# Performance work log

Hardware: AMD Instinct MI355X
Metric: run time of the kernel (lower is better)

Reference implementation:

```python
import jax, jax.numpy as jnp
import numpy as np

N_A, N_G, D, H = 100000, 25000, 128, 4
E_B, E_O, E_R, E_P = 400000, 100000, 200000, 200000
BN_INV = float(1.0 / np.sqrt(1.0 + 1e-5))  # eval-mode BatchNorm1d, running mean 0 / var 1


def setup_inputs():
    key = jax.random.key(0)
    ks = iter(jax.random.split(key, 64))
    nrm = lambda shape, s=0.05: jax.random.normal(next(ks), shape, jnp.float32) * s
    ri = lambda n, hi: jax.random.randint(next(ks), (n,), 0, hi, jnp.int32)
    inp = dict(
        x_atom=nrm((N_A, D), 1.0), x_group=nrm((N_G, D), 1.0),
        ef_bond=nrm((E_B, D), 1.0), ef_overlap=nrm((E_O, D), 1.0),
        bond_src=ri(E_B, N_A), bond_dst=ri(E_B, N_A),
        ov_src=ri(E_O, N_G), ov_dst=ri(E_O, N_G),
        ref_src=ri(E_R, N_G), ref_dst=ri(E_R, N_A),
        pool_src=ri(E_P, N_A), pool_dst=ri(E_P, N_G),
    )
    # two GINE convs (bond 'b', overlap 'o'): eps + MLP Linear(D,2D)->BN->ReLU->Linear(2D,D)
    for pre in ('b', 'o'):
        inp[pre + '_eps'] = jnp.zeros((1,), jnp.float32)
        inp[pre + '_W1'] = nrm((D, 2 * D)); inp[pre + '_b1'] = jnp.zeros((2 * D,), jnp.float32)
        inp[pre + '_g1'] = jnp.ones((2 * D,), jnp.float32); inp[pre + '_be1'] = jnp.zeros((2 * D,), jnp.float32)
        inp[pre + '_W2'] = nrm((2 * D, D)); inp[pre + '_b2'] = jnp.zeros((D,), jnp.float32)
    # two ModifiedGATConvs (refine 'r', pool 'p'): GATConv + Flatten->BN->ReLU->Linear
    for pre in ('r', 'p'):
        inp[pre + '_Wfc'] = nrm((D, H * D)); inp[pre + '_al'] = nrm((H, D)); inp[pre + '_ar'] = nrm((H, D))
        inp[pre + '_Wres'] = nrm((D, H * D)); inp[pre + '_bias'] = jnp.zeros((H * D,), jnp.float32)
        inp[pre + '_g'] = jnp.ones((H * D,), jnp.float32); inp[pre + '_b'] = jnp.zeros((H * D,), jnp.float32)
        inp[pre + '_Wout'] = nrm((H * D, D)); inp[pre + '_bout'] = jnp.zeros((D,), jnp.float32)
    return inp


def _gine(x_src, x_dst, efeat, src, dst, n_dst, eps, W1, b1, g1, be1, W2, b2):
    m = jax.nn.relu(x_src[src] + efeat)                       # [E, D] message: relu(h_src + e)
    neigh = jax.ops.segment_sum(m, dst, num_segments=n_dst)   # [Nd, D] sum-reduce
    h = (1.0 + eps) * x_dst + neigh
    h = h @ W1 + b1
    h = jax.nn.relu(g1 * (h * BN_INV) + be1)                  # eval BN
    return h @ W2 + b2


def _gat(x_src, x_dst, src, dst, n_dst, Wfc, al, ar, Wres, bias, g, b, Wout, bout):
    hs = (x_src @ Wfc).reshape(-1, H, D)                      # [Ns, H, D]
    hd = (x_dst @ Wfc).reshape(-1, H, D)
    el = jnp.sum(hs * al, axis=-1)                            # [Ns, H]
    er = jnp.sum(hd * ar, axis=-1)                            # [Nd, H]
    e = jax.nn.leaky_relu(el[src] + er[dst], 0.2)             # [E, H]
    emax = jax.ops.segment_max(e, dst, num_segments=n_dst)    # per-dst softmax (stable)
    ex = jnp.exp(e - emax[dst])
    den = jax.ops.segment_sum(ex, dst, num_segments=n_dst)
    a = ex / jnp.maximum(den[dst], 1e-9)                      # [E, H]
    rst = jax.ops.segment_sum(a[:, :, None] * hs[src], dst, num_segments=n_dst)  # [Nd, H, D]
    rst = rst + (x_dst @ Wres).reshape(-1, H, D) + bias.reshape(H, D)            # residual + bias
    flat = rst.reshape(-1, H * D)                             # Flatten
    h = jax.nn.relu(g * (flat * BN_INV) + b)                  # eval BN -> ReLU
    return h @ Wout + bout


def reference(x_atom, x_group, ef_bond, ef_overlap, bond_src, bond_dst, ov_src, ov_dst, ref_src, ref_dst, pool_src, pool_dst, b_eps, b_W1, b_b1, b_g1, b_be1, b_W2, b_b2, o_eps, o_W1, o_b1, o_g1, o_be1, o_W2, o_b2, r_Wfc, r_al, r_ar, r_Wres, r_bias, r_g, r_b, r_Wout, r_bout, p_Wfc, p_al, p_ar, p_Wres, p_bias, p_g, p_b, p_Wout, p_bout):
    # HeteroGraphConv with default 'sum' cross-relation aggregation per dst node type
    out_atom = _gine(x_atom, x_atom, ef_bond, bond_src, bond_dst, N_A, b_eps, b_W1, b_b1, b_g1, b_be1, b_W2, b_b2)
    out_atom = out_atom + _gat(x_group, x_atom, ref_src, ref_dst, N_A, r_Wfc, r_al, r_ar, r_Wres, r_bias, r_g, r_b, r_Wout, r_bout)
    out_group = _gine(x_group, x_group, ef_overlap, ov_src, ov_dst, N_G, o_eps, o_W1, o_b1, o_g1, o_be1, o_W2, o_b2)
    out_group = out_group + _gat(x_atom, x_group, pool_src, pool_dst, N_G, p_Wfc, p_al, p_ar, p_Wres, p_bias, p_g, p_b, p_Wout, p_bout)
    return jnp.concatenate([out_atom, out_group], axis=0)     # [N_A + N_G, D]
```

## Files before the change

### kernel.cpp

```cpp
#include <hip/hip_runtime.h>
#include <hip/hip_bf16.h>

#define N_A 100000
#define N_G 25000
#define DD 128
#define E_B 400000
#define E_O 100000
#define E_R 200000
#define E_P 200000
#define EALL 900000
#define NSLOT 250000
#define STRIDE 64
#define NALL 125000
#define GBN 7813

static constexpr float BN_INV_C = 0.99999500003749969f;

typedef __attribute__((ext_vector_type(8))) short bf16x8;
typedef __attribute__((ext_vector_type(4))) float f32x4;

__device__ __forceinline__ unsigned short f2bf(float f) {
    unsigned u = __float_as_uint(f);
    unsigned r = (u + 0x7FFFu + ((u >> 16) & 1u)) >> 16;
    return (unsigned short)r;
}
__device__ __forceinline__ float bf2f(unsigned short s) {
    return __uint_as_float(((unsigned)s) << 16);
}
__device__ __forceinline__ float lrelu(float v) { return v > 0.f ? v : 0.2f * v; }

__device__ __forceinline__ void gload16(const unsigned short* g, unsigned short* l) {
    __builtin_amdgcn_global_load_lds(
        (const __attribute__((address_space(1))) void*)g,
        (__attribute__((address_space(3))) void*)l, 16, 0, 0);
}

struct WcSeg { const float* src; unsigned short* dst; int K; int N; int ldk; int off; };
struct PrepArgs {
    const float* xa; const float* xg;
    unsigned short* xab; unsigned short* xgb;
    WcSeg wc[10];
    const float* rWfc; const float* ral; const float* rar;
    const float* pWfc; const float* pal; const float* par;
    float* wv;
    const int* bs; const int* bd; const int* os; const int* od;
    const int* rs; const int* rd; const int* ps; const int* pd;
    int* deg; uint2* adj; int* heads; int* nxt;
};

#define PB_XC 15625
#define PB_WC 2560
#define PB_WAR 8

__global__ __launch_bounds__(256) void k_prep(PrepArgs p) {
    int bx = blockIdx.x, tid = threadIdx.x;
    if (bx < PB_XC) {
        int t = bx * 256 + tid;
        if (t < N_A * 32) {
            float4 v = *(const float4*)(p.xa + (size_t)t * 4);
            ushort4 o; o.x = f2bf(v.x); o.y = f2bf(v.y); o.z = f2bf(v.z); o.w = f2bf(v.w);
            *(ushort4*)(p.xab + (size_t)t * 4) = o;
        } else {
            int t2 = t - N_A * 32;
            if (t2 < N_G * 32) {
                float4 v = *(const float4*)(p.xg + (size_t)t2 * 4);
                ushort4 o; o.x = f2bf(v.x); o.y = f2bf(v.y); o.z = f2bf(v.z); o.w = f2bf(v.w);
                *(ushort4*)(p.xgb + (size_t)t2 * 4) = o;
            }
        }
    } else if (bx < PB_XC + PB_WC) {
        int b2 = bx - PB_XC;
        WcSeg sg = p.wc[b2 >> 8];
        int t = ((b2 & 255) << 8) + tid;
        if (t < sg.K * sg.N) {
            int n = t % sg.N, k = t / sg.N;
            sg.dst[(size_t)n * sg.ldk + sg.off + k] = f2bf(sg.src[t]);
        }
    } else if (bx < PB_XC + PB_WC + PB_WAR) {
        int b3 = bx - (PB_XC + PB_WC);
        int bsel = b3 >> 1;
        int t = ((b3 & 1) << 8) + tid;
        const float* W = bsel < 2 ? p.rWfc : p.pWfc;
        const float* vec = bsel == 0 ? p.ral : bsel == 1 ? p.rar : bsel == 2 ? p.pal : p.par;
        int k = t >> 2, h = t & 3;
        const float* wr = W + (size_t)k * 512 + h * 128;
        const float* av = vec + h * 128;
        float s = 0.f;
        for (int d = 0; d < 128; ++d) s += wr[d] * av[d];
        p.wv[bsel * 512 + t] = s;
    } else {
        int t = (bx - (PB_XC + PB_WC + PB_WAR)) * 256 + tid;
        int e, base, go; const int* S; const int* D;
        if (t < E_B) { e = t; S = p.bs; D = p.bd; base = 0; go = 0; }
        else if (t < E_B + E_O) { e = t - E_B; S = p.os; D = p.od; base = 100000; go = E_B; }
        else if (t < E_B + E_O + E_R) { e = t - (E_B + E_O); S = p.rs; D = p.rd; base = 125000; go = E_B + E_O; }
        else if (t < EALL) { e = t - (E_B + E_O + E_R); S = p.ps; D = p.pd; base = 225000; go = E_B + E_O + E_R; }
        else return;
        int d = D[e], s = S[e];
        int ns = base + d;
        int pos = atomicAdd(&p.deg[ns], 1);
        if (pos < STRIDE) p.adj[(size_t)ns * STRIDE + pos] = make_uint2((unsigned)e, (unsigned)s);
        else p.nxt[go + e] = atomicExch(&p.heads[ns], e);
    }
}

__device__ __forceinline__ void gine16_body(
    int bx, int tid,
    const unsigned short* __restrict__ xAb, const unsigned short* __restrict__ xGb,
    const float* __restrict__ efB, const float* __restrict__ efO,
    const int* __restrict__ bsrc, const int* __restrict__ osrc,
    const int* __restrict__ deg, const uint2* __restrict__ adj,
    const int* __restrict__ heads, const int* __restrict__ nxt,
    const float* __restrict__ beps, const float* __restrict__ oeps,
    unsigned short* __restrict__ h0A, unsigned short* __restrict__ h0G,
    uint2* glbuf, int* degb) {
    int wid = tid >> 6, lane = tid & 63;
    int half = lane >> 5, l32 = lane & 31;
    int nbase = bx * 16 + wid * 4;
    bool atomside = nbase < N_A;
    const unsigned short* xs = atomside ? xAb : xGb;
    const float* ef = atomside ? efB : efO;
    const int* esrc = atomside ? bsrc : osrc;
    const int* nx = atomside ? nxt : nxt + E_B;
    float ep = 1.0f + (atomside ? beps[0] : oeps[0]);
    unsigned short* h0 = atomside ? h0A : h0G;
    uint2* glw = glbuf + wid * 4 * STRIDE;
#pragma unroll
    for (int j = 0; j < 4; ++j) {
        int nj = nbase + j;
        if (nj < NALL) glw[j * STRIDE + lane] = adj[(size_t)nj * STRIDE + lane];
    }
    if (lane < 4) {
        int nj = nbase + lane;
        degb[wid * 4 + lane] = (nj < NALL) ? deg[nj] : 0;
    }
    __syncthreads();
    for (int j = 0; j < 4; ++j) {
        int nj = nbase + j;
        if (nj >= NALL) break;
        int dd = degb[wid * 4 + j];
        int cb = min(dd, STRIDE);
        int nn = atomside ? nj : nj - N_A;
        const uint2* gl = glw + j * STRIDE;
        float4 acc = make_float4(0.f, 0.f, 0.f, 0.f);
        int i = 0;
        for (; i + 4 <= cb; i += 4) {
            uint2 eA = gl[i + half];
            uint2 eB = gl[i + 2 + half];
            uint2 xwA = *(const uint2*)(xs + (size_t)eA.y * DD + l32 * 4);
            float4 evA = *(const float4*)(ef + (size_t)eA.x * DD + l32 * 4);
            uint2 xwB = *(const uint2*)(xs + (size_t)eB.y * DD + l32 * 4);
            float4 evB = *(const float4*)(ef + (size_t)eB.x * DD + l32 * 4);
            acc.x += fmaxf(bf2f((unsigned short)(xwA.x & 0xffff)) + evA.x, 0.f);
            acc.y += fmaxf(bf2f((unsigned short)(xwA.x >> 16)) + evA.y, 0.f);
            acc.z += fmaxf(bf2f((unsigned short)(xwA.y & 0xffff)) + evA.z, 0.f);
            acc.w += fmaxf(bf2f((unsigned short)(xwA.y >> 16)) + evA.w, 0.f);
            acc.x += fmaxf(bf2f((unsigned short)(xwB.x & 0xffff)) + evB.x, 0.f);
            acc.y += fmaxf(bf2f((unsigned short)(xwB.x >> 16)) + evB.y, 0.f);
            acc.z += fmaxf(bf2f((unsigned short)(xwB.y & 0xffff)) + evB.z, 0.f);
            acc.w += fmaxf(bf2f((unsigned short)(xwB.y >> 16)) + evB.w, 0.f);
        }
        for (; i + 2 <= cb; i += 2) {
            uint2 eA = gl[i + half];
            uint2 xwA = *(const uint2*)(xs + (size_t)eA.y * DD + l32 * 4);
            float4 evA = *(const float4*)(ef + (size_t)eA.x * DD + l32 * 4);
            acc.x += fmaxf(bf2f((unsigned short)(xwA.x & 0xffff)) + evA.x, 0.f);
            acc.y += fmaxf(bf2f((unsigned short)(xwA.x >> 16)) + evA.y, 0.f);
            acc.z += fmaxf(bf2f((unsigned short)(xwA.y & 0xffff)) + evA.z, 0.f);
            acc.w += fmaxf(bf2f((unsigned short)(xwA.y >> 16)) + evA.w, 0.f);
        }
        if (i < cb && half == 0) {
            uint2 eA = gl[i];
            uint2 xwA = *(const uint2*)(xs + (size_t)eA.y * DD + l32 * 4);
            float4 evA = *(const float4*)(ef + (size_t)eA.x * DD + l32 * 4);
            acc.x += fmaxf(bf2f((unsigned short)(xwA.x & 0xffff)) + evA.x, 0.f);
            acc.y += fmaxf(bf2f((unsigned short)(xwA.x >> 16)) + evA.y, 0.f);
            acc.z += fmaxf(bf2f((unsigned short)(xwA.y & 0xffff)) + evA.z, 0.f);
            acc.w += fmaxf(bf2f((unsigned short)(xwA.y >> 16)) + evA.w, 0.f);
        }
        if (dd > STRIDE && half == 0) {
            for (int e = heads[nj]; e >= 0; e = nx[e]) {
                int s = esrc[e];
                uint2 xwA = *(const uint2*)(xs + (size_t)s * DD + l32 * 4);
                float4 evA = *(const float4*)(ef + (size_t)e * DD + l32 * 4);
                acc.x += fmaxf(bf2f((unsigned short)(xwA.x & 0xffff)) + evA.x, 0.f);
                acc.y += fmaxf(bf2f((unsigned short)(xwA.x >> 16)) + evA.y, 0.f);
                acc.z += fmaxf(bf2f((unsigned short)(xwA.y & 0xffff)) + evA.z, 0.f);
                acc.w += fmaxf(bf2f((unsigned short)(xwA.y >> 16)) + evA.w, 0.f);
            }
        }
        acc.x += __shfl_xor(acc.x, 32, 64);
        acc.y += __shfl_xor(acc.y, 32, 64);
        acc.z += __shfl_xor(acc.z, 32, 64);
        acc.w += __shfl_xor(acc.w, 32, 64);
        uint2 xd = *(const uint2*)(xs + (size_t)nn * DD + l32 * 4);
        float r0 = ep * bf2f((unsigned short)(xd.x & 0xffff)) + acc.x;
        float r1 = ep * bf2f((unsigned short)(xd.x >> 16)) + acc.y;
        float r2 = ep * bf2f((unsigned short)(xd.y & 0xffff)) + acc.z;
        float r3 = ep * bf2f((unsigned short)(xd.y >> 16)) + acc.w;
        if (half == 0) {
            uint2 o;
            o.x = (unsigned)f2bf(r0) | ((unsigned)f2bf(r1) << 16);
            o.y = (unsigned)f2bf(r2) | ((unsigned)f2bf(r3) << 16);
            *(uint2*)(h0 + (size_t)nn * DD + l32 * 4) = o;
        }
    }
}

__device__ __forceinline__ void logit_body(
    int t,
    const unsigned short* __restrict__ xAb, const unsigned short* __restrict__ xGb,
    const float* __restrict__ wv,
    float* __restrict__ elR, float* __restrict__ elP,
    float* __restrict__ erR, float* __restrict__ erP) {
    const unsigned short* xr; const float* wl; const float* wr_; float* ol; float* orr; int idx;
    if (t < N_A * 4) {
        idx = t; xr = xAb + (size_t)(t >> 2) * DD; wl = wv + 1024; wr_ = wv + 512;
        ol = elP; orr = erR;
    } else {
        int t2 = t - N_A * 4;
        if (t2 >= N_G * 4) return;
        idx = t2; xr = xGb + (size_t)(t2 >> 2) * DD; wl = wv; wr_ = wv + 1536;
        ol = elR; orr = erP;
    }
    int h = idx & 3;
    float sl = 0.f, sr = 0.f;
#pragma unroll
    for (int k = 0; k < DD; k += 8) {
        uint4 w = *(const uint4*)(xr + k);
        unsigned wa[4] = {w.x, w.y, w.z, w.w};
#pragma unroll
        for (int q = 0; q < 4; ++q) {
            float x0 = bf2f((unsigned short)(wa[q] & 0xffff));
            float x1 = bf2f((unsigned short)(wa[q] >> 16));
            int k0 = (k + q * 2) * 4 + h, k1 = (k + q * 2 + 1) * 4 + h;
            sl += x0 * wl[k0] + x1 * wl[k1];
            sr += x0 * wr_[k0] + x1 * wr_[k1];
        }
    }
    ol[idx] = sl;
    orr[idx] = sr;
}

__global__ __launch_bounds__(256) void k_gather_logit(
    const unsigned short* __restrict__ xAb, const unsigned short* __restrict__ xGb,
    const float* __restrict__ efB, const float* __restrict__ efO,
    const int* __restrict__ bsrc, const int* __restrict__ osrc,
    const int* __restrict__ deg, const uint2* __restrict__ adj,
    const int* __restrict__ heads, const int* __restrict__ nxt,
    const float* __restrict__ beps, const float* __restrict__ oeps,
    unsigned short* __restrict__ h0A, unsigned short* __restrict__ h0G,
    const float* __restrict__ wv,
    float* __restrict__ elR, float* __restrict__ elP,
    float* __restrict__ erR, float* __restrict__ erP) {
    __shared__ uint2 gl[16 * STRIDE];
    __shared__ int degb[16];
    int bx = blockIdx.x;
    if (bx < GBN)
        gine16_body(bx, threadIdx.x, xAb, xGb, efB, efO, bsrc, osrc, deg, adj, heads, nxt,
                    beps, oeps, h0A, h0G, gl, degb);
    else
        logit_body((bx - GBN) * 256 + threadIdx.x, xAb, xGb, wv, elR, elP, erR, erP);
}

__device__ __forceinline__ void exp_body(
    int t,
    const float* __restrict__ elR, const float* __restrict__ erR,
    const float* __restrict__ elP, const float* __restrict__ erP,
    const int* __restrict__ rs, const int* __restrict__ rd,
    const int* __restrict__ ps, const int* __restrict__ pd,
    float* __restrict__ exR, float* __restrict__ exP,
    float* __restrict__ denR, float* __restrict__ denP) {
    if (t < E_R * 4) {
        int e = t >> 2, h = t & 3;
        float v = lrelu(elR[rs[e] * 4 + h] + erR[rd[e] * 4 + h]);
        float x = __expf(v);
        exR[t] = x;
        atomicAdd(&denR[rd[e] * 4 + h], x);
    } else {
        int t2 = t - E_R * 4;
        if (t2 >= E_P * 4) return;
        int e = t2 >> 2, h = t2 & 3;
        float v = lrelu(elP[ps[e] * 4 + h] + erP[pd[e] * 4 + h]);
        float x = __expf(v);
        exP[t2] = x;
        atomicAdd(&denP[pd[e] * 4 + h], x);
    }
}

__global__ __launch_bounds__(256) void k_att_gather_all(
    const unsigned short* __restrict__ xAb, const unsigned short* __restrict__ xGb,
    const float* __restrict__ exR, const float* __restrict__ exP,
    const float* __restrict__ denR, const float* __restrict__ denP,
    const int* __restrict__ rsrc, const int* __restrict__ psrc,
    const int* __restrict__ deg, const uint2* __restrict__ adj,
    const int* __restrict__ heads, const int* __restrict__ nxt,
    unsigned short* __restrict__ A2r, unsigned short* __restrict__ A2p) {
    __shared__ uint2 glbuf[16 * STRIDE];
    __shared__ int degb[16];
    int tid = threadIdx.x;
    int wid = tid >> 6, lane = tid & 63;
    int half = lane >> 5, l32 = lane & 31;
    int nbase = blockIdx.x * 16 + wid * 4;
    bool atomside = nbase < N_A;
    const unsigned short* xs = atomside ? xGb : xAb;
    const float* ex = atomside ? exR : exP;
    const float* den = atomside ? denR : denP;
    const int* esrc = atomside ? rsrc : psrc;
    const int* nx = atomside ? nxt + (E_B + E_O) : nxt + (E_B + E_O + E_R);
    unsigned short* A2b = atomside ? A2r : A2p;
    uint2* glw = glbuf + wid * 4 * STRIDE;
#pragma unroll
    for (int j = 0; j < 4; ++j) {
        int nj = nbase + j;
        if (nj < NALL) glw[j * STRIDE + lane] = adj[(size_t)(125000 + nj) * STRIDE + lane];
    }
    if (lane < 4) {
        int nj = nbase + lane;
        degb[wid * 4 + lane] = (nj < NALL) ? deg[125000 + nj] : 0;
    }
    __syncthreads();
    for (int j = 0; j < 4; ++j) {
        int nj = nbase + j;
        if (nj >= NALL) break;
        int dd = degb[wid * 4 + j];
        int cb = min(dd, STRIDE);
        int nn = atomside ? nj : nj - N_A;
        const uint2* gl = glw + j * STRIDE;
        unsigned short* A2 = A2b + (size_t)nn * 512;
        float4 dv = *(const float4*)(den + (size_t)nn * 4);
        float inv0 = 1.f / fmaxf(dv.x, 1e-9f);
        float inv1 = 1.f / fmaxf(dv.y, 1e-9f);
        float inv2 = 1.f / fmaxf(dv.z, 1e-9f);
        float inv3 = 1.f / fmaxf(dv.w, 1e-9f);
        float acc[4][4] = {};
        int i = 0;
#define ATT_EDGE(e4_, xw_) { \
        float x0 = bf2f((unsigned short)(xw_.x & 0xffff)); \
        float x1 = bf2f((unsigned short)(xw_.x >> 16)); \
        float x2 = bf2f((unsigned short)(xw_.y & 0xffff)); \
        float x3 = bf2f((unsigned short)(xw_.y >> 16)); \
        float a0 = e4_.x * inv0, a1 = e4_.y * inv1, a2 = e4_.z * inv2, a3 = e4_.w * inv3; \
        acc[0][0] += a0 * x0; acc[0][1] += a0 * x1; acc[0][2] += a0 * x2; acc[0][3] += a0 * x3; \
        acc[1][0] += a1 * x0; acc[1][1] += a1 * x1; acc[1][2] += a1 * x2; acc[1][3] += a1 * x3; \
        acc[2][0] += a2 * x0; acc[2][1] += a2 * x1; acc[2][2] += a2 * x2; acc[2][3] += a2 * x3; \
        acc[3][0] += a3 * x0; acc[3][1] += a3 * x1; acc[3][2] += a3 * x2; acc[3][3] += a3 * x3; }
        for (; i + 4 <= cb; i += 4) {
            uint2 eA = gl[i + half], eB = gl[i + 2 + half];
            float4 e4A = *(const float4*)(ex + (size_t)eA.x * 4);
            uint2 xwA = *(const uint2*)(xs + (size_t)eA.y * DD + l32 * 4);
            float4 e4B = *(const float4*)(ex + (size_t)eB.x * 4);
            uint2 xwB = *(const uint2*)(xs + (size_t)eB.y * DD + l32 * 4);
            ATT_EDGE(e4A, xwA);
            ATT_EDGE(e4B, xwB);
        }
        for (; i + 2 <= cb; i += 2) {
            uint2 eA = gl[i + half];
            float4 e4A = *(const float4*)(ex + (size_t)eA.x * 4);
            uint2 xwA = *(const uint2*)(xs + (size_t)eA.y * DD + l32 * 4);
            ATT_EDGE(e4A, xwA);
        }
        if (i < cb && half == 0) {
            uint2 eA = gl[i];
            float4 e4A = *(const float4*)(ex + (size_t)eA.x * 4);
            uint2 xwA = *(const uint2*)(xs + (size_t)eA.y * DD + l32 * 4);
            ATT_EDGE(e4A, xwA);
        }
        if (dd > STRIDE && half == 0) {
            for (int e = heads[125000 + nj]; e >= 0; e = nx[e]) {
                int s = esrc[e];
                float4 e4A = *(const float4*)(ex + (size_t)e * 4);
                uint2 xwA = *(const uint2*)(xs + (size_t)s * DD + l32 * 4);
                ATT_EDGE(e4A, xwA);
            }
        }
#undef ATT_EDGE
#pragma unroll
        for (int h = 0; h < 4; ++h)
#pragma unroll
            for (int q = 0; q < 4; ++q)
                acc[h][q] += __shfl_xor(acc[h][q], 32, 64);
        if (half == 0) {
#pragma unroll
            for (int h = 0; h < 4; ++h) {
                uint2 o;
                o.x = (unsigned)f2bf(acc[h][0]) | ((unsigned)f2bf(acc[h][1]) << 16);
                o.y = (unsigned)f2bf(acc[h][2]) | ((unsigned)f2bf(acc[h][3]) << 16);
                *(uint2*)(A2 + h * 128 + l32 * 4) = o;
            }
        }
    }
}

template <int EPI, int OUTBF, int GATK>
__device__ __forceinline__ void gemm_body(
    const unsigned short* __restrict__ A, const unsigned short* __restrict__ Bt,
    void* __restrict__ C, int M, int N, int K,
    const float* __restrict__ bias, const float* __restrict__ g,
    const float* __restrict__ be, const unsigned short* __restrict__ addbf,
    const unsigned short* __restrict__ Axd, int bxx, int byy,
    unsigned short* As, unsigned short* Bs) {
    int tid = threadIdx.x;
    int wave = tid >> 6, lane = tid & 63;
    int wr = wave >> 1, wc = wave & 1;
    int row0 = byy * 128, col0 = bxx * 128;
    int l16 = lane & 15, q = lane >> 4;
    int r0s = wave * 16 + (lane >> 2);
    int r1s = r0s + 64;
    int swl = (lane ^ (lane >> 2) ^ (lane >> 4)) & 3;
    int swr = (l16 ^ (l16 >> 2)) & 3;
    unsigned short* ldsA0 = As + wave * 512;
    unsigned short* ldsA1 = As + 2048 + wave * 512;
    unsigned short* ldsB0 = Bs + wave * 512;
    unsigned short* ldsB1 = Bs + 2048 + wave * 512;
    f32x4 acc[4][4] = {};
    for (int k0 = 0; k0 < K; k0 += 32) {
        __syncthreads();
        {
            int kk = k0 + swl * 8;
            int ra0 = min(row0 + r0s, M - 1);
            int ra1 = min(row0 + r1s, M - 1);
            const unsigned short *pa0, *pa1;
            if (GATK) {
                if (k0 < 128) {
                    pa0 = A + (size_t)ra0 * 512 + col0 + kk;
                    pa1 = A + (size_t)ra1 * 512 + col0 + kk;
                } else {
                    pa0 = Axd + (size_t)ra0 * 128 + (kk - 128);
                    pa1 = Axd + (size_t)ra1 * 128 + (kk - 128);
                }
            } else {
                pa0 = A + (size_t)ra0 * K + kk;
                pa1 = A + (size_t)ra1 * K + kk;
            }
            gload16(pa0, ldsA0);
            gload16(pa1, ldsA1);
            gload16(Bt + (size_t)(col0 + r0s) * K + kk, ldsB0);
            gload16(Bt + (size_t)(col0 + r1s) * K + kk, ldsB1);
        }
        __syncthreads();
        bf16x8 af[4], bfr[4];
#pragma unroll
        for (int i = 0; i < 4; ++i) {
            int row = wr * 64 + i * 16 + l16;
            af[i] = *(const bf16x8*)(&As[row * 32 + ((q ^ swr) * 8)]);
        }
#pragma unroll
        for (int j = 0; j < 4; ++j) {
            int row = wc * 64 + j * 16 + l16;
            bfr[j] = *(const bf16x8*)(&Bs[row * 32 + ((q ^ swr) * 8)]);
        }
#pragma unroll
        for (int i = 0; i < 4; ++i)
#pragma unroll
            for (int j = 0; j < 4; ++j)
                acc[i][j] = __builtin_amdgcn_mfma_f32_16x16x32_bf16(af[i], bfr[j], acc[i][j], 0, 0, 0);
    }
    int rq = (lane >> 4) * 4;
#pragma unroll
    for (int i = 0; i < 4; ++i) {
#pragma unroll
        for (int reg = 0; reg < 4; ++reg) {
            int r = row0 + wr * 64 + i * 16 + rq + reg;
            if (r >= M) continue;
#pragma unroll
            for (int j = 0; j < 4; ++j) {
                int c = col0 + wc * 64 + j * 16 + l16;
                float v = acc[i][j][reg];
                size_t idx = (size_t)r * N + c;
                v += bias[c];
                if (EPI == 2) {
                    v = g[c] * (v * BN_INV_C) + be[c];
                    v = fmaxf(v, 0.f);
                }
                if (EPI == 3) {
                    ((float*)C)[idx] = v + bf2f(addbf[idx]);
                } else if (OUTBF) {
                    ((unsigned short*)C)[idx] = f2bf(v);
                } else {
                    ((float*)C)[idx] = v;
                }
            }
        }
    }
}

#define NBA 782
#define NBG 196

__global__ __launch_bounds__(256) void k_gemm1_exp(
    const unsigned short* h0A, const unsigned short* h0G,
    const unsigned short* WtB1, const unsigned short* WtO1,
    const float* bb1, const float* bg1, const float* bbe1,
    const float* ob1, const float* og1, const float* obe1,
    unsigned short* R4a, unsigned short* R4g,
    const float* elR, const float* erR, const float* elP, const float* erP,
    const int* rs, const int* rd, const int* ps, const int* pd,
    float* exR, float* exP, float* denR, float* denP) {
    __shared__ unsigned short As[4096];
    __shared__ unsigned short Bs[4096];
    int b = blockIdx.x;
    if (b < 2 * NBA)
        gemm_body<2, 1, 0>(h0A, WtB1, R4a, N_A, 256, 128, bb1, bg1, bbe1, nullptr, nullptr,
                           b & 1, b >> 1, As, Bs);
    else if (b < 2 * NBA + 2 * NBG) {
        int b2 = b - 2 * NBA;
        gemm_body<2, 1, 0>(h0G, WtO1, R4g, N_G, 256, 128, ob1, og1, obe1, nullptr, nullptr,
                           b2 & 1, b2 >> 1, As, Bs);
    } else {
        int t = (b - (2 * NBA + 2 * NBG)) * 256 + threadIdx.x;
        exp_body(t, elR, erR, elP, erP, rs, rd, ps, pd, exR, exP, denR, denP);
    }
}

__global__ __launch_bounds__(256) void k_gatk_mid(
    const unsigned short* R4a, const unsigned short* R4g,
    const unsigned short* WtB2, const unsigned short* WtO2,
    const float* bb2, const float* ob2,
    unsigned short* G1a, unsigned short* G1g,
    const unsigned short* A2r, const unsigned short* A2p,
    const unsigned short* xAb, const unsigned short* xGb,
    const unsigned short* WtR, const unsigned short* WtP,
    const float* rbias, const float* rg, const float* rb,
    const float* pbias, const float* pg, const float* pb,
    unsigned short* R3r, unsigned short* R3p) {
    __shared__ unsigned short As[4096];
    __shared__ unsigned short Bs[4096];
    int b = blockIdx.x;
    if (b < NBA)
        gemm_body<1, 1, 0>(R4a, WtB2, G1a, N_A, 128, 256, bb2, nullptr, nullptr, nullptr, nullptr,
                           0, b, As, Bs);
    else if (b < NBA + NBG)
        gemm_body<1, 1, 0>(R4g, WtO2, G1g, N_G, 128, 256, ob2, nullptr, nullptr, nullptr, nullptr,
                           0, b - NBA, As, Bs);
    else if (b < NBA + NBG + 4 * NBA) {
        int b3 = b - (NBA + NBG);
        gemm_body<2, 1, 1>(A2r, WtR, R3r, N_A, 512, 256, rbias, rg, rb, nullptr, xAb,
                           b3 & 3, b3 >> 2, As, Bs);
    } else {
        int b4 = b - (NBA + NBG + 4 * NBA);
        gemm_body<2, 1, 1>(A2p, WtP, R3p, N_G, 512, 256, pbias, pg, pb, nullptr, xGb,
                           b4 & 3, b4 >> 2, As, Bs);
    }
}

__global__ __launch_bounds__(256) void k_gemm_out(
    const unsigned short* R3r, const unsigned short* R3p,
    const unsigned short* WtRo, const unsigned short* WtPo,
    const float* rbout, const float* pbout,
    const unsigned short* G1a, const unsigned short* G1g,
    float* out) {
    __shared__ unsigned short As[4096];
    __shared__ unsigned short Bs[4096];
    int b = blockIdx.x;
    if (b < NBA)
        gemm_body<3, 0, 0>(R3r, WtRo, out, N_A, 128, 512, rbout, nullptr, nullptr, G1a, nullptr,
                           0, b, As, Bs);
    else
        gemm_body<3, 0, 0>(R3p, WtPo, out + (size_t)N_A * DD, N_G, 128, 512, pbout, nullptr, nullptr,
                           G1g, nullptr, 0, b - NBA, As, Bs);
}

extern "C" void kernel_launch(void* const* d_in, const int* in_sizes, int n_in,
                              void* d_out, int out_size, void* d_ws, size_t ws_size,
                              hipStream_t stream) {
    const float* x_atom = (const float*)d_in[0];
    const float* x_group = (const float*)d_in[1];
    const float* ef_bond = (const float*)d_in[2];
    const float* ef_ov = (const float*)d_in[3];
    const int* bond_src = (const int*)d_in[4];
    const int* bond_dst = (const int*)d_in[5];
    const int* ov_src = (const int*)d_in[6];
    const int* ov_dst = (const int*)d_in[7];
    const int* ref_src = (const int*)d_in[8];
    const int* ref_dst = (const int*)d_in[9];
    const int* pool_src = (const int*)d_in[10];
    const int* pool_dst = (const int*)d_in[11];
    const float* b_eps = (const float*)d_in[12];
    const float* b_W1 = (const float*)d_in[13];
    const float* b_b1 = (const float*)d_in[14];
    const float* b_g1 = (const float*)d_in[15];
    const float* b_be1 = (const float*)d_in[16];
    const float* b_W2 = (const float*)d_in[17];
    const float* b_b2 = (const float*)d_in[18];
    const float* o_eps = (const float*)d_in[19];
    const float* o_W1 = (const float*)d_in[20];
    const float* o_b1 = (const float*)d_in[21];
    const float* o_g1 = (const float*)d_in[22];
    const float* o_be1 = (const float*)d_in[23];
    const float* o_W2 = (const float*)d_in[24];
    const float* o_b2 = (const float*)d_in[25];
    const float* r_Wfc = (const float*)d_in[26];
    const float* r_al = (const float*)d_in[27];
    const float* r_ar = (const float*)d_in[28];
    const float* r_Wres = (const float*)d_in[29];
    const float* r_bias = (const float*)d_in[30];
    const float* r_g = (const float*)d_in[31];
    const float* r_b = (const float*)d_in[32];
    const float* r_Wout = (const float*)d_in[33];
    const float* r_bout = (const float*)d_in[34];
    const float* p_Wfc = (const float*)d_in[35];
    const float* p_al = (const float*)d_in[36];
    const float* p_ar = (const float*)d_in[37];
    const float* p_Wres = (const float*)d_in[38];
    const float* p_bias = (const float*)d_in[39];
    const float* p_g = (const float*)d_in[40];
    const float* p_b = (const float*)d_in[41];
    const float* p_Wout = (const float*)d_in[42];
    const float* p_bout = (const float*)d_in[43];

    float* out = (float*)d_out;
    char* wsb = (char*)d_ws;
    unsigned short* xAb = (unsigned short*)(wsb + 0);
    unsigned short* xGb = (unsigned short*)(wsb + 26000000);
    unsigned short* WtB1 = (unsigned short*)(wsb + 33000000);
    unsigned short* WtB2 = WtB1 + 32768;
    unsigned short* WtO1 = WtB2 + 32768;
    unsigned short* WtO2 = WtO1 + 32768;
    unsigned short* WtR  = WtO2 + 32768;
    unsigned short* WtRo = WtR + 131072;
    unsigned short* WtP  = WtRo + 65536;
    unsigned short* WtPo = WtP + 131072;
    float* wv   = (float*)(wsb + 34100000);
    int* heads  = (int*)(wsb + 36300000);
    int* nxt    = (int*)(wsb + 37400000);
    unsigned short* h0A = (unsigned short*)(wsb + 41100000);
    unsigned short* h0G = (unsigned short*)(wsb + 66800000);
    unsigned short* R4a = (unsigned short*)(wsb + 73300000);
    unsigned short* G1a = (unsigned short*)(wsb + 124600000);
    unsigned short* G1g = (unsigned short*)(wsb + 150300000);
    unsigned short* A2r = (unsigned short*)(wsb + 156800000);
    unsigned short* A2p = (unsigned short*)(wsb + 259300000);
    unsigned short* R3r = (unsigned short*)(wsb + 285000000);
    unsigned short* R3p = (unsigned short*)(wsb + 387500000);
    uint2* adj  = (uint2*)(wsb + 414000000);
    int* deg    = (int*)(wsb + 543000000);
    float* F    = (float*)(wsb + 544000000);
    float* elR  = F;
    float* elP  = F + 100000;
    float* erR  = F + 500000;
    float* erP  = F + 900000;
    float* denR = F + 1000000;
    float* denP = F + 1400000;
    float* exR  = F + 1500000;
    float* exP  = F + 2300000;
    unsigned short* R4g = (unsigned short*)(wsb + 560000000);

    hipMemsetAsync(deg, 0, NSLOT * 4, stream);
    hipMemsetAsync(heads, 0xFF, NSLOT * 4, stream);
    hipMemsetAsync(denR, 0, 500000 * 4, stream);

    PrepArgs pa;
    pa.xa = x_atom; pa.xg = x_group; pa.xab = xAb; pa.xgb = xGb;
    pa.wc[0] = {b_W1, WtB1, 128, 256, 128, 0};
    pa.wc[1] = {b_W2, WtB2, 256, 128, 256, 0};
    pa.wc[2] = {o_W1, WtO1, 128, 256, 128, 0};
    pa.wc[3] = {o_W2, WtO2, 256, 128, 256, 0};
    pa.wc[4] = {r_Wfc, WtR, 128, 512, 256, 0};
    pa.wc[5] = {r_Wres, WtR, 128, 512, 256, 128};
    pa.wc[6] = {r_Wout, WtRo, 512, 128, 512, 0};
    pa.wc[7] = {p_Wfc, WtP, 128, 512, 256, 0};
    pa.wc[8] = {p_Wres, WtP, 128, 512, 256, 128};
    pa.wc[9] = {p_Wout, WtPo, 512, 128, 512, 0};
    pa.rWfc = r_Wfc; pa.ral = r_al; pa.rar = r_ar;
    pa.pWfc = p_Wfc; pa.pal = p_al; pa.par = p_ar; pa.wv = wv;
    pa.bs = bond_src; pa.bd = bond_dst; pa.os = ov_src; pa.od = ov_dst;
    pa.rs = ref_src; pa.rd = ref_dst; pa.ps = pool_src; pa.pd = pool_dst;
    pa.deg = deg; pa.adj = adj; pa.heads = heads; pa.nxt = nxt;
    k_prep<<<PB_XC + PB_WC + PB_WAR + 3516, 256, 0, stream>>>(pa);

    k_gather_logit<<<GBN + 1954, 256, 0, stream>>>(
        xAb, xGb, ef_bond, ef_ov, bond_src, ov_src, deg, adj, heads, nxt,
        b_eps, o_eps, h0A, h0G, wv, elR, elP, erR, erP);

    k_gemm1_exp<<<2 * NBA + 2 * NBG + 6250, 256, 0, stream>>>(
        h0A, h0G, WtB1, WtO1, b_b1, b_g1, b_be1, o_b1, o_g1, o_be1, R4a, R4g,
        elR, erR, elP, erP, ref_src, ref_dst, pool_src, pool_dst, exR, exP, denR, denP);

    k_att_gather_all<<<GBN, 256, 0, stream>>>(
        xAb, xGb, exR, exP, denR, denP, ref_src, pool_src, deg, adj, heads, nxt, A2r, A2p);

    k_gatk_mid<<<NBA + NBG + 4 * NBA + 4 * NBG, 256, 0, stream>>>(
        R4a, R4g, WtB2, WtO2, b_b2, o_b2, G1a, G1g,
        A2r, A2p, xAb, xGb, WtR, WtP,
        r_bias, r_g, r_b, p_bias, p_g, p_b, R3r, R3p);

    k_gemm_out<<<NBA + NBG, 256, 0, stream>>>(R3r, R3p, WtRo, WtPo, r_bout, p_bout,
                                              G1a, G1g, out);
}
```

Measured before the change: 528.2 us.

## Process four nodes per wave in parallel with 16-lane groups in gathers

In both the GINE neighbor gather and the attention gather, each wave now splits into four 16-lane groups, each handling one destination node with 8 features per lane and 16-byte loads. Previously each wave walked its four nodes one after another, splitting each node's edges across two 32-lane halves and combining them with shuffles. The new scheme drops the cross-half shuffle reduction and serial node loop, giving more independent memory requests in flight. In exchange it uses more registers per lane (32 accumulators in attention) and causes divergence when node degrees differ within a wave.

Result: faster. 516.1 us (-2.3%).

```diff
diff --git a/kernel.cpp b/kernel.cpp
--- a/kernel.cpp
+++ b/kernel.cpp
@@ -104,6 +104,21 @@
     }
 }
 
+__device__ __forceinline__ void gine_acc(const unsigned short* __restrict__ xs,
+                                         const float* __restrict__ ef,
+                                         uint2 es, int l16, float* acc) {
+    uint4 xw = *(const uint4*)(xs + (size_t)es.y * DD + l16 * 8);
+    float4 e0 = *(const float4*)(ef + (size_t)es.x * DD + l16 * 8);
+    float4 e1 = *(const float4*)(ef + (size_t)es.x * DD + l16 * 8 + 4);
+    unsigned w[4] = {xw.x, xw.y, xw.z, xw.w};
+    float ev[8] = {e0.x, e0.y, e0.z, e0.w, e1.x, e1.y, e1.z, e1.w};
+#pragma unroll
+    for (int q = 0; q < 4; ++q) {
+        acc[q * 2]     += fmaxf(bf2f((unsigned short)(w[q] & 0xffff)) + ev[q * 2], 0.f);
+        acc[q * 2 + 1] += fmaxf(bf2f((unsigned short)(w[q] >> 16)) + ev[q * 2 + 1], 0.f);
+    }
+}
+
 __device__ __forceinline__ void gine16_body(
     int bx, int tid,
     const unsigned short* __restrict__ xAb, const unsigned short* __restrict__ xGb,
@@ -115,7 +130,7 @@
     unsigned short* __restrict__ h0A, unsigned short* __restrict__ h0G,
     uint2* glbuf, int* degb) {
     int wid = tid >> 6, lane = tid & 63;
-    int half = lane >> 5, l32 = lane & 31;
+    int grp = lane >> 4, l16 = lane & 15;
     int nbase = bx * 16 + wid * 4;
     bool atomside = nbase < N_A;
     const unsigned short* xs = atomside ? xAb : xGb;
@@ -135,76 +150,35 @@
         degb[wid * 4 + lane] = (nj < NALL) ? deg[nj] : 0;
     }
     __syncthreads();
-    for (int j = 0; j < 4; ++j) {
-        int nj = nbase + j;
-        if (nj >= NALL) break;
-        int dd = degb[wid * 4 + j];
-        int cb = min(dd, STRIDE);
-        int nn = atomside ? nj : nj - N_A;
-        const uint2* gl = glw + j * STRIDE;
-        float4 acc = make_float4(0.f, 0.f, 0.f, 0.f);
-        int i = 0;
-        for (; i + 4 <= cb; i += 4) {
-            uint2 eA = gl[i + half];
-            uint2 eB = gl[i + 2 + half];
-            uint2 xwA = *(const uint2*)(xs + (size_t)eA.y * DD + l32 * 4);
-            float4 evA = *(const float4*)(ef + (size_t)eA.x * DD + l32 * 4);
-            uint2 xwB = *(const uint2*)(xs + (size_t)eB.y * DD + l32 * 4);
-            float4 evB = *(const float4*)(ef + (size_t)eB.x * DD + l32 * 4);
-            acc.x += fmaxf(bf2f((unsigned short)(xwA.x & 0xffff)) + evA.x, 0.f);
-            acc.y += fmaxf(bf2f((unsigned short)(xwA.x >> 16)) + evA.y, 0.f);
-            acc.z += fmaxf(bf2f((unsigned short)(xwA.y & 0xffff)) + evA.z, 0.f);
-            acc.w += fmaxf(bf2f((unsigned short)(xwA.y >> 16)) + evA.w, 0.f);
-            acc.x += fmaxf(bf2f((unsigned short)(xwB.x & 0xffff)) + evB.x, 0.f);
-            acc.y += fmaxf(bf2f((unsigned short)(xwB.x >> 16)) + evB.y, 0.f);
-            acc.z += fmaxf(bf2f((unsigned short)(xwB.y & 0xffff)) + evB.z, 0.f);
-            acc.w += fmaxf(bf2f((unsigned short)(xwB.y >> 16)) + evB.w, 0.f);
-        }
-        for (; i + 2 <= cb; i += 2) {
-            uint2 eA = gl[i + half];
-            uint2 xwA = *(const uint2*)(xs + (size_t)eA.y * DD + l32 * 4);
-            float4 evA = *(const float4*)(ef + (size_t)eA.x * DD + l32 * 4);
-            acc.x += fmaxf(bf2f((unsigned short)(xwA.x & 0xffff)) + evA.x, 0.f);
-            acc.y += fmaxf(bf2f((unsigned short)(xwA.x >> 16)) + evA.y, 0.f);
-            acc.z += fmaxf(bf2f((unsigned short)(xwA.y & 0xffff)) + evA.z, 0.f);
-            acc.w += fmaxf(bf2f((unsigned short)(xwA.y >> 16)) + evA.w, 0.f);
-        }
-        if (i < cb && half == 0) {
-            uint2 eA = gl[i];
-            uint2 xwA = *(const uint2*)(xs + (size_t)eA.y * DD + l32 * 4);
-            float4 evA = *(const float4*)(ef + (size_t)eA.x * DD + l32 * 4);
-            acc.x += fmaxf(bf2f((unsigned short)(xwA.x & 0xffff)) + evA.x, 0.f);
-            acc.y += fmaxf(bf2f((unsigned short)(xwA.x >> 16)) + evA.y, 0.f);
-            acc.z += fmaxf(bf2f((unsigned short)(xwA.y & 0xffff)) + evA.z, 0.f);
-            acc.w += fmaxf(bf2f((unsigned short)(xwA.y >> 16)) + evA.w, 0.f);
-        }
-        if (dd > STRIDE && half == 0) {
-            for (int e = heads[nj]; e >= 0; e = nx[e]) {
-                int s = esrc[e];
-                uint2 xwA = *(const uint2*)(xs + (size_t)s * DD + l32 * 4);
-                float4 evA = *(const float4*)(ef + (size_t)e * DD + l32 * 4);
-                acc.x += fmaxf(bf2f((unsigned short)(xwA.x & 0xffff)) + evA.x, 0.f);
-                acc.y += fmaxf(bf2f((unsigned short)(xwA.x >> 16)) + evA.y, 0.f);
-                acc.z += fmaxf(bf2f((unsigned short)(xwA.y & 0xffff)) + evA.z, 0.f);
-                acc.w += fmaxf(bf2f((unsigned short)(xwA.y >> 16)) + evA.w, 0.f);
-            }
-        }
-        acc.x += __shfl_xor(acc.x, 32, 64);
-        acc.y += __shfl_xor(acc.y, 32, 64);
-        acc.z += __shfl_xor(acc.z, 32, 64);
-        acc.w += __shfl_xor(acc.w, 32, 64);
-        uint2 xd = *(const uint2*)(xs + (size_t)nn * DD + l32 * 4);
-        float r0 = ep * bf2f((unsigned short)(xd.x & 0xffff)) + acc.x;
-        float r1 = ep * bf2f((unsigned short)(xd.x >> 16)) + acc.y;
-        float r2 = ep * bf2f((unsigned short)(xd.y & 0xffff)) + acc.z;
-        float r3 = ep * bf2f((unsigned short)(xd.y >> 16)) + acc.w;
-        if (half == 0) {
-            uint2 o;
-            o.x = (unsigned)f2bf(r0) | ((unsigned)f2bf(r1) << 16);
-            o.y = (unsigned)f2bf(r2) | ((unsigned)f2bf(r3) << 16);
-            *(uint2*)(h0 + (size_t)nn * DD + l32 * 4) = o;
-        }
-    }
+    int nj = nbase + grp;
+    if (nj >= NALL) return;
+    int dd = degb[wid * 4 + grp];
+    int cb = min(dd, STRIDE);
+    int nn = atomside ? nj : nj - N_A;
+    const uint2* gl = glw + grp * STRIDE;
+    float acc[8] = {0.f, 0.f, 0.f, 0.f, 0.f, 0.f, 0.f, 0.f};
+    int i = 0;
+    for (; i + 2 <= cb; i += 2) {
+        gine_acc(xs, ef, gl[i], l16, acc);
+        gine_acc(xs, ef, gl[i + 1], l16, acc);
+    }
+    if (i < cb) gine_acc(xs, ef, gl[i], l16, acc);
+    if (dd > STRIDE) {
+        for (int e = heads[nj]; e >= 0; e = nx[e])
+            gine_acc(xs, ef, make_uint2((unsigned)e, (unsigned)esrc[e]), l16, acc);
+    }
+    uint4 xd = *(const uint4*)(xs + (size_t)nn * DD + l16 * 8);
+    unsigned w[4] = {xd.x, xd.y, xd.z, xd.w};
+    uint4 o;
+    unsigned ow[4];
+#pragma unroll
+    for (int q = 0; q < 4; ++q) {
+        float v0 = ep * bf2f((unsigned short)(w[q] & 0xffff)) + acc[q * 2];
+        float v1 = ep * bf2f((unsigned short)(w[q] >> 16)) + acc[q * 2 + 1];
+        ow[q] = (unsigned)f2bf(v0) | ((unsigned)f2bf(v1) << 16);
+    }
+    o.x = ow[0]; o.y = ow[1]; o.z = ow[2]; o.w = ow[3];
+    *(uint4*)(h0 + (size_t)nn * DD + l16 * 8) = o;
 }
 
 __device__ __forceinline__ void logit_body(
@@ -288,6 +262,26 @@
     }
 }
 
+__device__ __forceinline__ void att_acc(const unsigned short* __restrict__ xs,
+                                        const float* __restrict__ ex,
+                                        uint2 es, int l16, const float* inv,
+                                        float acc[4][8]) {
+    float4 e4 = *(const float4*)(ex + (size_t)es.x * 4);
+    uint4 xw = *(const uint4*)(xs + (size_t)es.y * DD + l16 * 8);
+    unsigned w[4] = {xw.x, xw.y, xw.z, xw.w};
+    float xv[8];
+#pragma unroll
+    for (int q = 0; q < 4; ++q) {
+        xv[q * 2] = bf2f((unsigned short)(w[q] & 0xffff));
+        xv[q * 2 + 1] = bf2f((unsigned short)(w[q] >> 16));
+    }
+    float a[4] = {e4.x * inv[0], e4.y * inv[1], e4.z * inv[2], e4.w * inv[3]};
+#pragma unroll
+    for (int h = 0; h < 4; ++h)
+#pragma unroll
+        for (int q = 0; q < 8; ++q) acc[h][q] += a[h] * xv[q];
+}
+
 __global__ __launch_bounds__(256) void k_att_gather_all(
     const unsigned short* __restrict__ xAb, const unsigned short* __restrict__ xGb,
     const float* __restrict__ exR, const float* __restrict__ exP,
@@ -300,7 +294,7 @@
     __shared__ int degb[16];
     int tid = threadIdx.x;
     int wid = tid >> 6, lane = tid & 63;
-    int half = lane >> 5, l32 = lane & 31;
+    int grp = lane >> 4, l16 = lane & 15;
     int nbase = blockIdx.x * 16 + wid * 4;
     bool atomside = nbase < N_A;
     const unsigned short* xs = atomside ? xGb : xAb;
@@ -320,75 +314,38 @@
         degb[wid * 4 + lane] = (nj < NALL) ? deg[125000 + nj] : 0;
     }
     __syncthreads();
-    for (int j = 0; j < 4; ++j) {
-        int nj = nbase + j;
-        if (nj >= NALL) break;
-        int dd = degb[wid * 4 + j];
-        int cb = min(dd, STRIDE);
-        int nn = atomside ? nj : nj - N_A;
-        const uint2* gl = glw + j * STRIDE;
-        unsigned short* A2 = A2b + (size_t)nn * 512;
-        float4 dv = *(const float4*)(den + (size_t)nn * 4);
-        float inv0 = 1.f / fmaxf(dv.x, 1e-9f);
-        float inv1 = 1.f / fmaxf(dv.y, 1e-9f);
-        float inv2 = 1.f / fmaxf(dv.z, 1e-9f);
-        float inv3 = 1.f / fmaxf(dv.w, 1e-9f);
-        float acc[4][4] = {};
-        int i = 0;
-#define ATT_EDGE(e4_, xw_) { \
-        float x0 = bf2f((unsigned short)(xw_.x & 0xffff)); \
-        float x1 = bf2f((unsigned short)(xw_.x >> 16)); \
-        float x2 = bf2f((unsigned short)(xw_.y & 0xffff)); \
-        float x3 = bf2f((unsigned short)(xw_.y >> 16)); \
-        float a0 = e4_.x * inv0, a1 = e4_.y * inv1, a2 = e4_.z * inv2, a3 = e4_.w * inv3; \
-        acc[0][0] += a0 * x0; acc[0][1] += a0 * x1; acc[0][2] += a0 * x2; acc[0][3] += a0 * x3; \
-        acc[1][0] += a1 * x0; acc[1][1] += a1 * x1; acc[1][2] += a1 * x2; acc[1][3] += a1 * x3; \
-        acc[2][0] += a2 * x0; acc[2][1] += a2 * x1; acc[2][2] += a2 * x2; acc[2][3] += a2 * x3; \
-        acc[3][0] += a3 * x0; acc[3][1] += a3 * x1; acc[3][2] += a3 * x2; acc[3][3] += a3 * x3; }
-        for (; i + 4 <= cb; i += 4) {
-            uint2 eA = gl[i + half], eB = gl[i + 2 + half];
-            float4 e4A = *(const float4*)(ex + (size_t)eA.x * 4);
-            uint2 xwA = *(const uint2*)(xs + (size_t)eA.y * DD + l32 * 4);
-            float4 e4B = *(const float4*)(ex + (size_t)eB.x * 4);
-            uint2 xwB = *(const uint2*)(xs + (size_t)eB.y * DD + l32 * 4);
-            ATT_EDGE(e4A, xwA);
-            ATT_EDGE(e4B, xwB);
-        }
-        for (; i + 2 <= cb; i += 2) {
-            uint2 eA = gl[i + half];
-            float4 e4A = *(const float4*)(ex + (size_t)eA.x * 4);
-            uint2 xwA = *(const uint2*)(xs + (size_t)eA.y * DD + l32 * 4);
-            ATT_EDGE(e4A, xwA);
-        }
-        if (i < cb && half == 0) {
-            uint2 eA = gl[i];
-            float4 e4A = *(const float4*)(ex + (size_t)eA.x * 4);
-            uint2 xwA = *(const uint2*)(xs + (size_t)eA.y * DD + l32 * 4);
-            ATT_EDGE(e4A, xwA);
-        }
-        if (dd > STRIDE && half == 0) {
-            for (int e = heads[125000 + nj]; e >= 0; e = nx[e]) {
-                int s = esrc[e];
-                float4 e4A = *(const float4*)(ex + (size_t)e * 4);
-                uint2 xwA = *(const uint2*)(xs + (size_t)s * DD + l32 * 4);
-                ATT_EDGE(e4A, xwA);
-            }
-        }
-#undef ATT_EDGE
-#pragma unroll
-        for (int h = 0; h < 4; ++h)
-#pragma unroll
-            for (int q = 0; q < 4; ++q)
-                acc[h][q] += __shfl_xor(acc[h][q], 32, 64);
-        if (half == 0) {
-#pragma unroll
-            for (int h = 0; h < 4; ++h) {
-                uint2 o;
-                o.x = (unsigned)f2bf(acc[h][0]) | ((unsigned)f2bf(acc[h][1]) << 16);
-                o.y = (unsigned)f2bf(acc[h][2]) | ((unsigned)f2bf(acc[h][3]) << 16);
-                *(uint2*)(A2 + h * 128 + l32 * 4) = o;
-            }
-        }
+    int nj = nbase + grp;
+    if (nj >= NALL) return;
+    int dd = degb[wid * 4 + grp];
+    int cb = min(dd, STRIDE);
+    int nn = atomside ? nj : nj - N_A;
+    const uint2* gl = glw + grp * STRIDE;
+    unsigned short* A2 = A2b + (size_t)nn * 512;
+    float4 dv = *(const float4*)(den + (size_t)nn * 4);
+    float inv[4];
+    inv[0] = 1.f / fmaxf(dv.x, 1e-9f);
+    inv[1] = 1.f / fmaxf(dv.y, 1e-9f);
+    inv[2] = 1.f / fmaxf(dv.z, 1e-9f);
+    inv[3] = 1.f / fmaxf(dv.w, 1e-9f);
+    float acc[4][8] = {};
+    int i = 0;
+    for (; i + 2 <= cb; i += 2) {
+        att_acc(xs, ex, gl[i], l16, inv, acc);
+        att_acc(xs, ex, gl[i + 1], l16, inv, acc);
+    }
+    if (i < cb) att_acc(xs, ex, gl[i], l16, inv, acc);
+    if (dd > STRIDE) {
+        for (int e = heads[125000 + nj]; e >= 0; e = nx[e])
+            att_acc(xs, ex, make_uint2((unsigned)e, (unsigned)esrc[e]), l16, inv, acc);
+    }
+#pragma unroll
+    for (int h = 0; h < 4; ++h) {
+        unsigned ow[4];
+#pragma unroll
+        for (int q = 0; q < 4; ++q)
+            ow[q] = (unsigned)f2bf(acc[h][q * 2]) | ((unsigned)f2bf(acc[h][q * 2 + 1]) << 16);
+        uint4 o; o.x = ow[0]; o.y = ow[1]; o.z = ow[2]; o.w = ow[3];
+        *(uint4*)(A2 + h * 128 + l16 * 8) = o;
     }
 }
 
```
